# Kernel optimization log

Hardware: AMD Instinct MI355X
Metric: run time of the kernel (lower is better)

The kernel has to match this reference:

```python
import jax, jax.numpy as jnp
import numpy as np

GAMMA = 0.2
ALPHA = 0.6

def setup_inputs() -> dict:
    key = jax.random.key(0)
    k1, k2 = jax.random.split(key)
    N, C = 262144, 160
    logits = jax.random.normal(k1, (N, C), dtype=jnp.float32)
    target = jax.random.randint(k2, (N, C), 0, 2, dtype=jnp.int32)
    return {"logits": logits, "target": target}

def reference(logits, target):
    # p = sigmoid(logits); per-element focal BCE, then mean-reduce.
    p = jax.nn.sigmoid(logits)
    pos = -ALPHA * (1.0 - p) ** GAMMA * jnp.log(p)
    neg = -(1.0 - ALPHA) * p ** GAMMA * jnp.log(1.0 - p)
    loss = jnp.where(target == 1, pos, neg)
    return loss.mean()
```

## Files before the change

kernel.cpp:

```cpp
#include <hip/hip_runtime.h>

#define GAMMA_C 0.2f

#define L2E_C 1.4426950408889634f
#define CPOS_C 0.41588830833596715f
#define CNEG_C 0.27725887222397810f

typedef float __attribute__((ext_vector_type(4))) f32x4;
typedef int   __attribute__((ext_vector_type(4))) i32x4;

__device__ __forceinline__ float focal_elem(float x, int t) {
    float xl = x * L2E_C;
    float e  = __builtin_amdgcn_exp2f(-xl);
    float s2 = __builtin_amdgcn_logf(1.0f + e);
    float a2 = xl + s2;
    bool ispos = (t == 1);
    float earg = ispos ? a2 : s2;
    float fac  = ispos ? s2 : a2;
    float cf   = ispos ? CPOS_C : CNEG_C;
    float ex   = __builtin_amdgcn_exp2f(-GAMMA_C * earg);
    return cf * fac * ex;
}

__device__ __forceinline__ float focal_vec4(f32x4 x4, i32x4 t4) {
    float r = focal_elem(x4.x, t4.x);
    r += focal_elem(x4.y, t4.y);
    r += focal_elem(x4.z, t4.z);
    r += focal_elem(x4.w, t4.w);
    return r;
}

__global__ __launch_bounds__(256) void focal_partial_kernel(
    const f32x4* __restrict__ logits4,
    const i32x4* __restrict__ target4,
    float* __restrict__ partial,
    long long nvec,
    const float* __restrict__ logits_s,
    const int* __restrict__ target_s,
    long long n)
{
    const long long chunk = (nvec + gridDim.x - 1) / gridDim.x;
    const long long start = (long long)blockIdx.x * chunk;
    long long end_ll = start + chunk;
    if (end_ll > nvec) end_ll = nvec;
    const int len = (int)(end_ll > start ? end_ll - start : 0);

    const f32x4* __restrict__ lg = logits4 + start;
    const i32x4* __restrict__ tg = target4 + start;

    float a0 = 0.0f, a1 = 0.0f, a2 = 0.0f, a3 = 0.0f;

    int k = threadIdx.x;
    for (; k + 1792 < len; k += 2048) {
        f32x4 x0 = lg[k];
        f32x4 x1 = lg[k + 256];
        f32x4 x2 = lg[k + 512];
        f32x4 x3 = lg[k + 768];
        f32x4 x4 = lg[k + 1024];
        f32x4 x5 = lg[k + 1280];
        f32x4 x6 = lg[k + 1536];
        f32x4 x7 = lg[k + 1792];
        i32x4 t0 = tg[k];
        i32x4 t1 = tg[k + 256];
        i32x4 t2 = tg[k + 512];
        i32x4 t3 = tg[k + 768];
        i32x4 t4 = tg[k + 1024];
        i32x4 t5 = tg[k + 1280];
        i32x4 t6 = tg[k + 1536];
        i32x4 t7 = tg[k + 1792];
        a0 += focal_vec4(x0, t0);
        a1 += focal_vec4(x1, t1);
        a2 += focal_vec4(x2, t2);
        a3 += focal_vec4(x3, t3);
        a0 += focal_vec4(x4, t4);
        a1 += focal_vec4(x5, t5);
        a2 += focal_vec4(x6, t6);
        a3 += focal_vec4(x7, t7);
    }
    for (; k < len; k += 256)
        a0 += focal_vec4(lg[k], tg[k]);

    float acc = (a0 + a1) + (a2 + a3);

    if (blockIdx.x == 0 && threadIdx.x == 0) {
        for (long long q = nvec * 4; q < n; ++q)
            acc += focal_elem(logits_s[q], target_s[q]);
    }

#pragma unroll
    for (int off = 32; off > 0; off >>= 1)
        acc += __shfl_down(acc, off, 64);

    __shared__ float smem[4];
    int lane = threadIdx.x & 63;
    int wid  = threadIdx.x >> 6;
    if (lane == 0) smem[wid] = acc;
    __syncthreads();
    if (threadIdx.x == 0)
        partial[blockIdx.x] = smem[0] + smem[1] + smem[2] + smem[3];
}

__global__ __launch_bounds__(256) void focal_final_kernel(
    const float* __restrict__ partial,
    int nblocks,
    float inv_count,
    float* __restrict__ out)
{
    float acc = 0.0f;
    for (int i = threadIdx.x; i < nblocks; i += 256)
        acc += partial[i];

#pragma unroll
    for (int off = 32; off > 0; off >>= 1)
        acc += __shfl_down(acc, off, 64);

    __shared__ float smem[4];
    int lane = threadIdx.x & 63;
    int wid  = threadIdx.x >> 6;
    if (lane == 0) smem[wid] = acc;
    __syncthreads();
    if (threadIdx.x == 0)
        out[0] = (smem[0] + smem[1] + smem[2] + smem[3]) * inv_count;
}

extern "C" void kernel_launch(void* const* d_in, const int* in_sizes, int n_in,
                              void* d_out, int out_size, void* d_ws, size_t ws_size,
                              hipStream_t stream) {
    const float* logits = (const float*)d_in[0];
    const int*   target = (const int*)d_in[1];
    long long n = (long long)in_sizes[0];
    long long nvec = n / 4;

    float* partial = (float*)d_ws;
    const int nblocks = 1024;
    const int nthreads = 256;

    focal_partial_kernel<<<nblocks, nthreads, 0, stream>>>(
        (const f32x4*)logits, (const i32x4*)target, partial, nvec,
        logits, target, n);
    focal_final_kernel<<<1, nthreads, 0, stream>>>(
        partial, nblocks, 1.0f / (float)n, (float*)d_out);
}
```

Measured before the change: 60.16 us.

## Fuse final reduction into main kernel via fixed-point atomics and last-block counter

The separate single-block final-reduction kernel is removed. Each block now converts its partial sum to a 64-bit fixed-point integer and atomically adds it into a global accumulator. A counter atomic lets the last block write the mean, and a small memset clears the workspace before launch. This saves one kernel launch and the partial-array round trip, but adds a memset operation and relies on atomic ordering between the sum and the counter.

```diff
diff --git a/kernel.cpp b/kernel.cpp
--- a/kernel.cpp
+++ b/kernel.cpp
@@ -5,6 +5,9 @@
 #define L2E_C 1.4426950408889634f
 #define CPOS_C 0.41588830833596715f
 #define CNEG_C 0.27725887222397810f
+
+#define FP_SCALE 1073741824.0f
+#define FP_INV_SCALE 9.31322574615478515625e-10
 
 typedef float __attribute__((ext_vector_type(4))) f32x4;
 typedef int   __attribute__((ext_vector_type(4))) i32x4;
@@ -30,14 +33,16 @@
     return r;
 }
 
-__global__ __launch_bounds__(256) void focal_partial_kernel(
+__global__ __launch_bounds__(256) void focal_fused_kernel(
     const f32x4* __restrict__ logits4,
     const i32x4* __restrict__ target4,
-    float* __restrict__ partial,
+    unsigned long long* __restrict__ fpsum,
+    unsigned* __restrict__ ctr,
     long long nvec,
     const float* __restrict__ logits_s,
     const int* __restrict__ target_s,
-    long long n)
+    long long n,
+    float* __restrict__ out)
 {
     const long long chunk = (nvec + gridDim.x - 1) / gridDim.x;
     const long long start = (long long)blockIdx.x * chunk;
@@ -92,35 +97,24 @@
         acc += __shfl_down(acc, off, 64);
 
     __shared__ float smem[4];
+    __shared__ bool is_last;
     int lane = threadIdx.x & 63;
     int wid  = threadIdx.x >> 6;
     if (lane == 0) smem[wid] = acc;
     __syncthreads();
-    if (threadIdx.x == 0)
-        partial[blockIdx.x] = smem[0] + smem[1] + smem[2] + smem[3];
-}
 
-__global__ __launch_bounds__(256) void focal_final_kernel(
-    const float* __restrict__ partial,
-    int nblocks,
-    float inv_count,
-    float* __restrict__ out)
-{
-    float acc = 0.0f;
-    for (int i = threadIdx.x; i < nblocks; i += 256)
-        acc += partial[i];
-
-#pragma unroll
-    for (int off = 32; off > 0; off >>= 1)
-        acc += __shfl_down(acc, off, 64);
-
-    __shared__ float smem[4];
-    int lane = threadIdx.x & 63;
-    int wid  = threadIdx.x >> 6;
-    if (lane == 0) smem[wid] = acc;
-    __syncthreads();
-    if (threadIdx.x == 0)
-        out[0] = (smem[0] + smem[1] + smem[2] + smem[3]) * inv_count;
+    if (threadIdx.x == 0) {
+        float bsum = smem[0] + smem[1] + smem[2] + smem[3];
+        unsigned long long q =
+            (unsigned long long)(long long)rintf(bsum * FP_SCALE);
+        unsigned long long old = atomicAdd(fpsum, q);
+        asm volatile("" :: "v"(old));
+        unsigned prev = atomicAdd(ctr, 1u);
+        if (prev == gridDim.x - 1u) {
+            unsigned long long total = atomicAdd(fpsum, 0ull);
+            out[0] = (float)((double)total * FP_INV_SCALE / (double)n);
+        }
+    }
 }
 
 extern "C" void kernel_launch(void* const* d_in, const int* in_sizes, int n_in,
@@ -131,13 +125,13 @@
     long long n = (long long)in_sizes[0];
     long long nvec = n / 4;
 
-    float* partial = (float*)d_ws;
+    unsigned long long* fpsum = (unsigned long long*)d_ws;
+    unsigned* ctr = (unsigned*)((char*)d_ws + 8);
     const int nblocks = 1024;
     const int nthreads = 256;
 
-    focal_partial_kernel<<<nblocks, nthreads, 0, stream>>>(
-        (const f32x4*)logits, (const i32x4*)target, partial, nvec,
-        logits, target, n);
-    focal_final_kernel<<<1, nthreads, 0, stream>>>(
-        partial, nblocks, 1.0f / (float)n, (float*)d_out);
+    hipMemsetAsync(d_ws, 0, 16, stream);
+    focal_fused_kernel<<<nblocks, nthreads, 0, stream>>>(
+        (const f32x4*)logits, (const i32x4*)target, fpsum, ctr, nvec,
+        logits, target, n, (float*)d_out);
 }
```

Result: slower. 70.93 us (+17.9%).
